# Kernel optimization log

Hardware: AMD Instinct MI355X
Metric: run time of the kernel (lower is better)

## Reference

```python
import jax, jax.numpy as jnp
import numpy as np

# Constants from the keras-fsaf repo this layer comes from
STRIDES = (8, 16, 32, 64, 128)
POS_SCALE = 0.2
IGNORE_SCALE = 0.5
IMAGE_SIZE = 1024
FEATURE_SHAPES = tuple((IMAGE_SIZE // s, IMAGE_SIZE // s) for s in STRIDES)  # (128,128)...(8,8)
NUM_CLASSES = 80
BATCH = 16
MAX_GT = 64
BIG_AREA = 1e7


def _prop_box(proj_boxes, scale, fw, fh):
    """Shrink projected boxes around their center by `scale`, round outward, clip."""
    x1, y1, x2, y2 = proj_boxes[:, 0], proj_boxes[:, 1], proj_boxes[:, 2], proj_boxes[:, 3]
    w, h = x2 - x1, y2 - y1
    a = (1.0 - scale) * 0.5
    nx1 = jnp.floor(x1 + a * w)
    ny1 = jnp.floor(y1 + a * h)
    nx2 = jnp.ceil(x2 - a * w)
    ny2 = jnp.ceil(y2 - a * h)
    nx2 = jnp.clip(jnp.maximum(nx2, nx1 + 1.0), 0.0, float(fw))
    ny2 = jnp.clip(jnp.maximum(ny2, ny1 + 1.0), 0.0, float(fh))
    nx1 = jnp.clip(nx1, 0.0, float(fw - 1))
    ny1 = jnp.clip(ny1, 0.0, float(fh - 1))
    return (nx1.astype(jnp.int32), ny1.astype(jnp.int32),
            nx2.astype(jnp.int32), ny2.astype(jnp.int32))


def _level_targets(levels, boxes, labels, level_id, stride, fh, fw):
    """Vectorized (over gt boxes) FSAF targets for one pyramid level of one image.
    levels:(N,) int, boxes:(N,4) float image coords, labels:(N,) int.
    """
    valid = (levels == level_id)  # (N,)
    proj = boxes / stride
    px1, py1, px2, py2 = _prop_box(proj, POS_SCALE, fw, fh)
    ix1, iy1, ix2, iy2 = _prop_box(proj, IGNORE_SCALE, fw, fh)

    ys = jnp.arange(fh, dtype=jnp.int32)
    xs = jnp.arange(fw, dtype=jnp.int32)

    def region(x1, y1, x2, y2):  # -> (N, fh, fw) bool
        iny = (ys[None, :, None] >= y1[:, None, None]) & (ys[None, :, None] < y2[:, None, None])
        inx = (xs[None, None, :] >= x1[:, None, None]) & (xs[None, None, :] < x2[:, None, None])
        return iny & inx

    in_pos = region(px1, py1, px2, py2) & valid[:, None, None]
    in_ign = region(ix1, iy1, ix2, iy2) & valid[:, None, None]

    # (l+r)*(t+b) == gt box area -> constant per box; pad value 1e7 outside pos region
    area = (boxes[:, 2] - boxes[:, 0]) * (boxes[:, 3] - boxes[:, 1])  # (N,)
    area_map = jnp.where(in_pos, area[:, None, None], BIG_AREA)  # (N,fh,fw)
    chosen = jnp.argmin(area_map, axis=0)  # (fh,fw) min-area overlap resolution
    chosen_pos = jnp.take_along_axis(in_pos, chosen[None], axis=0)[0]  # (fh,fw)

    # cls mask values: 2 in pos, 0 in ignore ring, -1 elsewhere; invalid boxes -> -1
    m = jnp.where(in_pos, 2.0, jnp.where(in_ign, 0.0, -1.0))
    mx = jnp.max(m, axis=0)  # (fh,fw)
    cls_mask = (mx == 2.0) | (mx == -1.0)
    num_pos = jnp.sum((mx == 2.0).astype(jnp.float32))
    regr_mask = jnp.any(in_pos, axis=0)

    cb = boxes[chosen]  # (fh,fw,4)
    sx = (xs.astype(jnp.float32) + 0.5) * stride  # (fw,)
    sy = (ys.astype(jnp.float32) + 0.5) * stride  # (fh,)
    l = sx[None, :] - cb[..., 0]
    t = sy[:, None] - cb[..., 1]
    r = cb[..., 2] - sx[None, :]
    b = cb[..., 3] - sy[:, None]
    posf = chosen_pos.astype(jnp.float32)[..., None]
    regr_target = jnp.stack((l, t, r, b), axis=-1) * (0.25) * posf  # (fh,fw,4)

    cls_target = jax.nn.one_hot(labels[chosen], NUM_CLASSES, dtype=jnp.float32) * posf

    hw = fh * fw
    return (cls_target.reshape(hw, NUM_CLASSES), cls_mask.reshape(hw), num_pos,
            regr_target.reshape(hw, 4), regr_mask.reshape(hw))


def _image_targets(levels, gt):
    boxes = gt[:, :4]
    labels = gt[:, 4].astype(jnp.int32)
    cls_ts, cls_ms, nps, reg_ts, reg_ms = [], [], [], [], []
    for lid, (stride, (fh, fw)) in enumerate(zip(STRIDES, FEATURE_SHAPES)):
        ct, cm, npos, rt, rm = _level_targets(levels, boxes, labels, lid, float(stride), fh, fw)
        cls_ts.append(ct); cls_ms.append(cm); nps.append(npos)
        reg_ts.append(rt); reg_ms.append(rm)
    return (jnp.concatenate(cls_ts, 0), jnp.concatenate(cls_ms, 0),
            jnp.sum(jnp.stack(nps)), jnp.concatenate(reg_ts, 0), jnp.concatenate(reg_ms, 0))


def setup_inputs() -> dict:
    key = jax.random.key(0)
    k1, k2, k3, k4, k5 = jax.random.split(key, 5)
    cx = jax.random.uniform(k1, (BATCH, MAX_GT), minval=0.0, maxval=float(IMAGE_SIZE))
    cy = jax.random.uniform(k2, (BATCH, MAX_GT), minval=0.0, maxval=float(IMAGE_SIZE))
    wh = jax.random.uniform(k3, (BATCH, MAX_GT, 2), minval=16.0, maxval=512.0)
    x1 = jnp.clip(cx - wh[..., 0] * 0.5, 0.0, IMAGE_SIZE - 2.0)
    y1 = jnp.clip(cy - wh[..., 1] * 0.5, 0.0, IMAGE_SIZE - 2.0)
    x2 = jnp.clip(cx + wh[..., 0] * 0.5, x1 + 2.0, float(IMAGE_SIZE))
    y2 = jnp.clip(cy + wh[..., 1] * 0.5, y1 + 2.0, float(IMAGE_SIZE))
    labels = jax.random.randint(k4, (BATCH, MAX_GT), 0, NUM_CLASSES).astype(jnp.float32)
    batch_gt_boxes = jnp.stack((x1, y1, x2, y2, labels), axis=-1)  # (B, MAX_GT, 5)
    batch_gt_box_levels = jax.random.randint(k5, (BATCH, MAX_GT), 0, len(STRIDES)).astype(jnp.int32)
    feature_shapes = jnp.broadcast_to(jnp.array(FEATURE_SHAPES, dtype=jnp.int32),
                                      (BATCH, len(STRIDES), 2))
    return {"batch_gt_box_levels": batch_gt_box_levels,
            "batch_gt_boxes": batch_gt_boxes,
            "feature_shapes": feature_shapes}


def reference(batch_gt_box_levels, batch_gt_boxes, feature_shapes):
    # feature_shapes carried for interface fidelity; spatial sizes are static constants.
    cls_t, cls_m, num_pos, reg_t, reg_m = jax.vmap(_image_targets)(batch_gt_box_levels,
                                                                   batch_gt_boxes)
    return cls_t, cls_m, num_pos, reg_t, reg_m
```

## Files before the change

### kernel.cpp

```cpp
#include <hip/hip_runtime.h>


#define NPIX      21824
#define NBOX      64
#define BATCH     16
#define NUM_CLS   80
#define BIG_AREA  10000000.0f

#define CLSM_OFF  27934720
#define NUMP_OFF  28283904
#define REGT_OFF  28283920
#define REGM_OFF  29680656

__device__ __forceinline__ void prop_box(float x1, float y1, float x2, float y2,
                                         float a, float fwf, float fhf,
                                         int& ox1, int& oy1, int& ox2, int& oy2) {
    float w = __fsub_rn(x2, x1);
    float h = __fsub_rn(y2, y1);
    float nx1 = floorf(__fadd_rn(x1, __fmul_rn(a, w)));
    float ny1 = floorf(__fadd_rn(y1, __fmul_rn(a, h)));
    float nx2 = ceilf(__fsub_rn(x2, __fmul_rn(a, w)));
    float ny2 = ceilf(__fsub_rn(y2, __fmul_rn(a, h)));
    nx2 = fminf(fmaxf(fmaxf(nx2, __fadd_rn(nx1, 1.0f)), 0.0f), fwf);
    ny2 = fminf(fmaxf(fmaxf(ny2, __fadd_rn(ny1, 1.0f)), 0.0f), fhf);
    nx1 = fminf(fmaxf(nx1, 0.0f), fwf - 1.0f);
    ny1 = fminf(fmaxf(ny1, 0.0f), fhf - 1.0f);
    ox1 = (int)nx1; oy1 = (int)ny1; ox2 = (int)nx2; oy2 = (int)ny2;
}

__global__ __launch_bounds__(256) void fsaf_kernel(const int* __restrict__ levels,
                                                   const float* __restrict__ gt,
                                                   float* __restrict__ out) {
    const int img = blockIdx.y;
    const int bx  = blockIdx.x;
    const int tid = threadIdx.x;

    int level, loff, fwl;
    if      (bx < 64) { level = 0; loff = 0;     fwl = 7; }
    else if (bx < 80) { level = 1; loff = 16384; fwl = 6; }
    else if (bx < 84) { level = 2; loff = 20480; fwl = 5; }
    else if (bx == 84){ level = 3; loff = 21504; fwl = 4; }
    else              { level = 4; loff = 21760; fwl = 3; }

    const int   fw      = 1 << fwl;
    const float stride  = (float)(8 << level);
    const int   pixBase = bx << 8;
    const int   numPix  = min(256, NPIX - pixBase);

    __shared__ int   s_px1[NBOX], s_py1[NBOX], s_px2[NBOX], s_py2[NBOX];
    __shared__ int   s_ix1[NBOX], s_iy1[NBOX], s_ix2[NBOX], s_iy2[NBOX];
    __shared__ float s_area[NBOX];
    __shared__ float s_bx1[NBOX], s_by1[NBOX], s_bx2[NBOX], s_by2[NBOX];
    __shared__ int   s_lab[NBOX];
    __shared__ int   s_plab[256];

    if (tid < NBOX) {
        const int n = tid;
        const float* g = gt + (size_t)(img * NBOX + n) * 5;
        float bx1 = g[0], by1 = g[1], bx2 = g[2], by2 = g[3];
        int   lab = (int)g[4];
        bool  valid = (levels[img * NBOX + n] == level);

        s_bx1[n] = bx1; s_by1[n] = by1; s_bx2[n] = bx2; s_by2[n] = by2;
        s_lab[n] = lab;
        s_area[n] = (bx2 - bx1) * (by2 - by1);

        const float inv = 1.0f / stride;
        float px1 = bx1 * inv, py1 = by1 * inv, px2 = bx2 * inv, py2 = by2 * inv;
        const float fwf = (float)fw, fhf = (float)fw;

        int a1, b1, a2, b2;
        prop_box(px1, py1, px2, py2, 0.4f, fwf, fhf, a1, b1, a2, b2);
        if (!valid) { a2 = -1; }
        s_px1[n] = a1; s_py1[n] = b1; s_px2[n] = a2; s_py2[n] = b2;

        prop_box(px1, py1, px2, py2, 0.25f, fwf, fhf, a1, b1, a2, b2);
        if (!valid) { a2 = -1; }
        s_ix1[n] = a1; s_iy1[n] = b1; s_ix2[n] = a2; s_iy2[n] = b2;
    }
    __syncthreads();

    const int  p      = pixBase + tid;
    const bool active = tid < numPix;

    float best   = BIG_AREA;
    int   chosen = 0;
    bool  anyIgn = false;

    int x = 0, y = 0;
    if (active) {
        int local = p - loff;
        y = local >> fwl;
        x = local & (fw - 1);
        #pragma unroll 8
        for (int n = 0; n < NBOX; ++n) {
            bool inp = (y >= s_py1[n]) & (y < s_py2[n]) & (x >= s_px1[n]) & (x < s_px2[n]);
            bool ing = (y >= s_iy1[n]) & (y < s_iy2[n]) & (x >= s_ix1[n]) & (x < s_ix2[n]);
            anyIgn |= ing;
            float am = inp ? s_area[n] : BIG_AREA;
            bool better = am < best;
            best   = better ? am : best;
            chosen = better ? n  : chosen;
        }
    }
    const bool anyPos = best < BIG_AREA;

    const size_t imgBase = (size_t)img * NPIX;
    if (active) {
        out[CLSM_OFF + imgBase + p] = (anyPos || !anyIgn) ? 1.0f : 0.0f;
        out[REGM_OFF + imgBase + p] = anyPos ? 1.0f : 0.0f;

        float4 rt = {0.f, 0.f, 0.f, 0.f};
        if (anyPos) {
            float sx = ((float)x + 0.5f) * stride;
            float sy = ((float)y + 0.5f) * stride;
            rt.x = (sx - s_bx1[chosen]) * 0.25f;
            rt.y = (sy - s_by1[chosen]) * 0.25f;
            rt.z = (s_bx2[chosen] - sx) * 0.25f;
            rt.w = (s_by2[chosen] - sy) * 0.25f;
        }
        ((float4*)out)[(size_t)REGT_OFF / 4 + imgBase + p] = rt;
    }
    s_plab[tid] = (active && anyPos) ? s_lab[chosen] : -1;

    unsigned long long bal = __ballot(active && anyPos);
    if ((tid & 63) == 0) {
        int c = __popcll(bal);
        if (c) atomicAdd(out + NUMP_OFF + img, (float)c);
    }
    __syncthreads();

    float4* cls4 = (float4*)out;
    const size_t base4 = (imgBase + (size_t)pixBase) * 20;
    const int total4 = numPix * 20;
    for (int f = tid; f < total4; f += 256) {
        int pix = f / 20;
        int c4  = f - pix * 20;
        int rel = s_plab[pix] - c4 * 4;
        float4 v = {0.f, 0.f, 0.f, 0.f};
        if      (rel == 0) v.x = 1.0f;
        else if (rel == 1) v.y = 1.0f;
        else if (rel == 2) v.z = 1.0f;
        else if (rel == 3) v.w = 1.0f;
        cls4[base4 + f] = v;
    }
}

extern "C" void kernel_launch(void* const* d_in, const int* in_sizes, int n_in,
                              void* d_out, int out_size, void* d_ws, size_t ws_size,
                              hipStream_t stream) {
    const int*   levels = (const int*)d_in[0];
    const float* gt     = (const float*)d_in[1];
    float*       out    = (float*)d_out;

    hipMemsetAsync((char*)d_out + (size_t)NUMP_OFF * sizeof(float), 0,
                   BATCH * sizeof(float), stream);

    dim3 grid(86, BATCH);
    fsaf_kernel<<<grid, 256, 0, stream>>>(levels, gt, out);
}
```

Baseline: 149.4 us.

## Cull boxes per block by level and row range, and scatter one-hot class targets

Each block now uses a wave ballot and prefix popcount to compact only the boxes that are valid for its level and whose ignore region overlaps its rows. The per-pixel overlap loop then runs over that short list instead of all 64 boxes. The class-target tensor is zero-filled with plain float4 stores at kernel start, and each positive pixel scatters a single 1.0, replacing the per-element divide-by-20 label decode and the shared label buffer. Box data is packed into int4 and float4 shared arrays. The cost is a scattered, uncoalesced store per positive pixel, and correctness depends on the block barrier ordering the zero fill before that store.

```diff
diff --git a/kernel.cpp b/kernel.cpp
--- a/kernel.cpp
+++ b/kernel.cpp
@@ -4,7 +4,6 @@
 #define NPIX      21824
 #define NBOX      64
 #define BATCH     16
-#define NUM_CLS   80
 #define BIG_AREA  10000000.0f
 
 #define CLSM_OFF  27934720
@@ -13,7 +12,7 @@
 #define REGM_OFF  29680656
 
 __device__ __forceinline__ void prop_box(float x1, float y1, float x2, float y2,
-                                         float a, float fwf, float fhf,
+                                         float a, float fwf,
                                          int& ox1, int& oy1, int& ox2, int& oy2) {
     float w = __fsub_rn(x2, x1);
     float h = __fsub_rn(y2, y1);
@@ -22,9 +21,9 @@
     float nx2 = ceilf(__fsub_rn(x2, __fmul_rn(a, w)));
     float ny2 = ceilf(__fsub_rn(y2, __fmul_rn(a, h)));
     nx2 = fminf(fmaxf(fmaxf(nx2, __fadd_rn(nx1, 1.0f)), 0.0f), fwf);
-    ny2 = fminf(fmaxf(fmaxf(ny2, __fadd_rn(ny1, 1.0f)), 0.0f), fhf);
+    ny2 = fminf(fmaxf(fmaxf(ny2, __fadd_rn(ny1, 1.0f)), 0.0f), fwf);
     nx1 = fminf(fmaxf(nx1, 0.0f), fwf - 1.0f);
-    ny1 = fminf(fmaxf(ny1, 0.0f), fhf - 1.0f);
+    ny1 = fminf(fmaxf(ny1, 0.0f), fwf - 1.0f);
     ox1 = (int)nx1; oy1 = (int)ny1; ox2 = (int)nx2; oy2 = (int)ny2;
 }
 
@@ -42,107 +41,101 @@
     else if (bx == 84){ level = 3; loff = 21504; fwl = 4; }
     else              { level = 4; loff = 21760; fwl = 3; }
 
-    const int   fw      = 1 << fwl;
-    const float stride  = (float)(8 << level);
-    const int   pixBase = bx << 8;
-    const int   numPix  = min(256, NPIX - pixBase);
+    const int    fw      = 1 << fwl;
+    const float  stride  = (float)(8 << level);
+    const int    pixBase = bx << 8;
+    const int    numPix  = min(256, NPIX - pixBase);
+    const size_t imgBase = (size_t)img * NPIX;
 
-    __shared__ int   s_px1[NBOX], s_py1[NBOX], s_px2[NBOX], s_py2[NBOX];
-    __shared__ int   s_ix1[NBOX], s_iy1[NBOX], s_ix2[NBOX], s_iy2[NBOX];
-    __shared__ float s_area[NBOX];
-    __shared__ float s_bx1[NBOX], s_by1[NBOX], s_bx2[NBOX], s_by2[NBOX];
-    __shared__ int   s_lab[NBOX];
-    __shared__ int   s_plab[256];
+    float4* cls4 = (float4*)out;
+    const size_t base4  = (imgBase + (size_t)pixBase) * 20;
+    const int    total4 = numPix * 20;
+    const float4 z4 = {0.f, 0.f, 0.f, 0.f};
+    for (int f = tid; f < total4; f += 256) cls4[base4 + f] = z4;
+
+    __shared__ int4   s_pos[NBOX];
+    __shared__ int4   s_ign[NBOX];
+    __shared__ float  s_area[NBOX];
+    __shared__ float4 s_box[NBOX];
+    __shared__ int    s_lab[NBOX];
+    __shared__ int    s_cnt;
 
     if (tid < NBOX) {
-        const int n = tid;
-        const float* g = gt + (size_t)(img * NBOX + n) * 5;
-        float bx1 = g[0], by1 = g[1], bx2 = g[2], by2 = g[3];
-        int   lab = (int)g[4];
-        bool  valid = (levels[img * NBOX + n] == level);
-
-        s_bx1[n] = bx1; s_by1[n] = by1; s_bx2[n] = bx2; s_by2[n] = by2;
-        s_lab[n] = lab;
-        s_area[n] = (bx2 - bx1) * (by2 - by1);
+        const float* g = gt + (size_t)(img * NBOX + tid) * 5;
+        float b0 = g[0], b1 = g[1], b2 = g[2], b3 = g[3];
+        int   lab   = (int)g[4];
+        bool  valid = (levels[img * NBOX + tid] == level);
 
         const float inv = 1.0f / stride;
-        float px1 = bx1 * inv, py1 = by1 * inv, px2 = bx2 * inv, py2 = by2 * inv;
-        const float fwf = (float)fw, fhf = (float)fw;
+        float px1 = b0 * inv, py1 = b1 * inv, px2 = b2 * inv, py2 = b3 * inv;
+        const float fwf = (float)fw;
 
-        int a1, b1, a2, b2;
-        prop_box(px1, py1, px2, py2, 0.4f, fwf, fhf, a1, b1, a2, b2);
-        if (!valid) { a2 = -1; }
-        s_px1[n] = a1; s_py1[n] = b1; s_px2[n] = a2; s_py2[n] = b2;
+        int pa, pb, pc, pd, ia, ib, ic, id;
+        prop_box(px1, py1, px2, py2, 0.4f,  fwf, pa, pb, pc, pd);
+        prop_box(px1, py1, px2, py2, 0.25f, fwf, ia, ib, ic, id);
 
-        prop_box(px1, py1, px2, py2, 0.25f, fwf, fhf, a1, b1, a2, b2);
-        if (!valid) { a2 = -1; }
-        s_ix1[n] = a1; s_iy1[n] = b1; s_ix2[n] = a2; s_iy2[n] = b2;
+        int y0   = (pixBase - loff) >> fwl;
+        int yEnd = y0 + (numPix >> fwl);
+        bool hit = valid && (ib < yEnd) && (id > y0);
+
+        unsigned long long m = __ballot(hit);
+        if (hit) {
+            int idx = __popcll(m & ((1ull << tid) - 1ull));
+            s_pos[idx]  = make_int4(pa, pb, pc, pd);
+            s_ign[idx]  = make_int4(ia, ib, ic, id);
+            s_area[idx] = (b2 - b0) * (b3 - b1);
+            s_box[idx]  = make_float4(b0, b1, b2, b3);
+            s_lab[idx]  = lab;
+        }
+        if (tid == 0) s_cnt = __popcll(m);
     }
     __syncthreads();
 
     const int  p      = pixBase + tid;
     const bool active = tid < numPix;
+    const int  local  = p - loff;
+    const int  y      = local >> fwl;
+    const int  x      = local & (fw - 1);
 
     float best   = BIG_AREA;
     int   chosen = 0;
     bool  anyIgn = false;
-
-    int x = 0, y = 0;
-    if (active) {
-        int local = p - loff;
-        y = local >> fwl;
-        x = local & (fw - 1);
-        #pragma unroll 8
-        for (int n = 0; n < NBOX; ++n) {
-            bool inp = (y >= s_py1[n]) & (y < s_py2[n]) & (x >= s_px1[n]) & (x < s_px2[n]);
-            bool ing = (y >= s_iy1[n]) & (y < s_iy2[n]) & (x >= s_ix1[n]) & (x < s_ix2[n]);
-            anyIgn |= ing;
-            float am = inp ? s_area[n] : BIG_AREA;
-            bool better = am < best;
-            best   = better ? am : best;
-            chosen = better ? n  : chosen;
-        }
+    const int cnt = s_cnt;
+    for (int n = 0; n < cnt; ++n) {
+        int4 ig = s_ign[n];
+        bool ing = (y >= ig.y) & (y < ig.w) & (x >= ig.x) & (x < ig.z);
+        anyIgn |= ing;
+        int4 ps = s_pos[n];
+        bool inp = (y >= ps.y) & (y < ps.w) & (x >= ps.x) & (x < ps.z);
+        float am = inp ? s_area[n] : BIG_AREA;
+        bool better = am < best;
+        best   = better ? am : best;
+        chosen = better ? n  : chosen;
     }
     const bool anyPos = best < BIG_AREA;
 
-    const size_t imgBase = (size_t)img * NPIX;
     if (active) {
         out[CLSM_OFF + imgBase + p] = (anyPos || !anyIgn) ? 1.0f : 0.0f;
         out[REGM_OFF + imgBase + p] = anyPos ? 1.0f : 0.0f;
 
-        float4 rt = {0.f, 0.f, 0.f, 0.f};
+        float4 rt = z4;
         if (anyPos) {
+            float4 cb = s_box[chosen];
             float sx = ((float)x + 0.5f) * stride;
             float sy = ((float)y + 0.5f) * stride;
-            rt.x = (sx - s_bx1[chosen]) * 0.25f;
-            rt.y = (sy - s_by1[chosen]) * 0.25f;
-            rt.z = (s_bx2[chosen] - sx) * 0.25f;
-            rt.w = (s_by2[chosen] - sy) * 0.25f;
+            rt.x = (sx - cb.x) * 0.25f;
+            rt.y = (sy - cb.y) * 0.25f;
+            rt.z = (cb.z - sx) * 0.25f;
+            rt.w = (cb.w - sy) * 0.25f;
+            out[(imgBase + p) * 80 + s_lab[chosen]] = 1.0f;
         }
         ((float4*)out)[(size_t)REGT_OFF / 4 + imgBase + p] = rt;
     }
-    s_plab[tid] = (active && anyPos) ? s_lab[chosen] : -1;
 
     unsigned long long bal = __ballot(active && anyPos);
     if ((tid & 63) == 0) {
         int c = __popcll(bal);
         if (c) atomicAdd(out + NUMP_OFF + img, (float)c);
-    }
-    __syncthreads();
-
-    float4* cls4 = (float4*)out;
-    const size_t base4 = (imgBase + (size_t)pixBase) * 20;
-    const int total4 = numPix * 20;
-    for (int f = tid; f < total4; f += 256) {
-        int pix = f / 20;
-        int c4  = f - pix * 20;
-        int rel = s_plab[pix] - c4 * 4;
-        float4 v = {0.f, 0.f, 0.f, 0.f};
-        if      (rel == 0) v.x = 1.0f;
-        else if (rel == 1) v.y = 1.0f;
-        else if (rel == 2) v.z = 1.0f;
-        else if (rel == 3) v.w = 1.0f;
-        cls4[base4 + f] = v;
     }
 }
 
```

New measurement: 140.3 us. 6.1% less time.
